# Optimization experiments

Hardware: AMD Instinct MI355X
Metric: run time of the kernel (lower is better)

Reference implementation:

```python
import jax, jax.numpy as jnp
import numpy as np

K = 9          # neighbors kept after dilation
DILATION = 2   # top-k runs with K*DILATION then strided slice
EPS = 1e-12    # F.normalize eps


def setup_inputs() -> dict:
    key = jax.random.key(0)
    # x: [B, C, N, 1] feature map over N points with C channels
    x = jax.random.normal(key, (2, 64, 8192, 1), dtype=jnp.float32)
    return {"x": x}


def reference(x):
    k_total = K * DILATION
    # L2-normalize along channel dim (F.normalize(x, p=2, dim=1))
    norm = jnp.sqrt(jnp.sum(x * x, axis=1, keepdims=True))
    xn = x / jnp.maximum(norm, EPS)
    # [B, C, N, 1] -> [B, N, C]
    pts = jnp.transpose(jnp.squeeze(xn, -1), (0, 2, 1))
    B, N, _ = pts.shape
    # pairwise squared distances: ||xi||^2 - 2 xi.xj + ||xj||^2  -> [B, N, N]
    sq = jnp.sum(pts * pts, axis=-1, keepdims=True)            # [B, N, 1]
    dist = sq - 2.0 * jnp.einsum('bnc,bmc->bnm', pts, pts) + jnp.swapaxes(sq, 1, 2)
    # k nearest = top-k of negated distance (matches torch.topk(-dist, k))
    _, nn_idx = jax.lax.top_k(-dist, k_total)                  # [B, N, k_total] int32
    center_idx = jnp.broadcast_to(jnp.arange(N, dtype=nn_idx.dtype)[None, :, None],
                                  (B, N, k_total))
    edge_index = jnp.stack([nn_idx, center_idx], axis=0)       # [2, B, N, k_total]
    # dilation (non-stochastic path): strided slice over neighbor dim
    return edge_index[:, :, :, ::DILATION]                     # [2, B, N, K]
```

## Files before the change

### kernel.cpp

```cpp
#include <hip/hip_runtime.h>


#define NPTS  8192
#define CHN   64
#define NB    2
#define KF    18
#define KC    8
#define KM    20
#define KOUT  9
#define NPART 4
#define TPB   32

typedef unsigned u32;
typedef unsigned short u16;
typedef unsigned long long u64;
typedef __attribute__((ext_vector_type(4))) unsigned u32x4;
typedef __attribute__((ext_vector_type(8))) short bf16x8;
typedef __attribute__((ext_vector_type(4))) float f32x4;

__device__ __forceinline__ u32 umin32(u32 a, u32 b) { return a < b ? a : b; }
__device__ __forceinline__ u32 umax32(u32 a, u32 b) { return a > b ? a : b; }

__device__ __forceinline__ u32 mono32(float f) {
  const u32 u = __float_as_uint(f);
  const u32 s = (u32)((int)u >> 31);
  return u ^ (s | 0x80000000u);
}

__device__ __forceinline__ u32 med3u(u32 a, u32 b, u32 c) {
  u32 r;
  asm("v_med3_u32 %0, %1, %2, %3" : "=v"(r) : "v"(a), "v"(b), "v"(c));
  return r;
}

template <int KK>
__device__ __forceinline__ void insmm(u32 key, u32 (&d)[KK]) {
#pragma unroll
  for (int k = KK - 1; k >= 1; --k) d[k] = med3u(d[k - 1], d[k], key);
  d[0] = umin32(d[0], key);
}

template <int KK>
__device__ __forceinline__ void ins64(u64 key, u64 (&d)[KK]) {
  if (key < d[KK - 1]) {
#pragma unroll
    for (int k = KK - 1; k >= 1; --k) {
      const bool up = d[k - 1] > key;
      const bool here = (!up) && (d[k] > key);
      d[k] = up ? d[k - 1] : (here ? key : d[k]);
    }
    if (d[0] > key) d[0] = key;
  }
}

__device__ __forceinline__ void gload_lds16(const u32* g, u32* l) {
  __builtin_amdgcn_global_load_lds(
      (const __attribute__((address_space(1))) u32*)g,
      (__attribute__((address_space(3))) u32*)l, 16, 0, 0);
}

__device__ __forceinline__ void np_normalize(const float* __restrict__ xb,
                                             float (&v)[CHN]) {
  float ss = 0.f;
#pragma unroll
  for (int c = 0; c < CHN; ++c) {
    v[c] = xb[(size_t)c * NPTS];
    ss = __fadd_rn(ss, __fmul_rn(v[c], v[c]));
  }
  const float den = fmaxf(__fsqrt_rn(ss), 1e-12f);
#pragma unroll
  for (int c = 0; c < CHN; ++c) v[c] = __fdiv_rn(v[c], den);
}

__global__ __launch_bounds__(128) void prep_kernel(
    const float* __restrict__ x, u32* __restrict__ hib, u32* __restrict__ lob,
    float* __restrict__ sq) {
  const int b = blockIdx.x >> 6;
  const int n = ((blockIdx.x & 63) << 7) + threadIdx.x;
  float v[CHN];
  np_normalize(x + (size_t)b * CHN * NPTS + n, v);
  float r[8];
#pragma unroll
  for (int j = 0; j < 8; ++j) r[j] = __fmul_rn(v[j], v[j]);
#pragma unroll
  for (int blk = 1; blk < 8; ++blk)
#pragma unroll
    for (int j = 0; j < 8; ++j)
      r[j] = __fadd_rn(r[j], __fmul_rn(v[8 * blk + j], v[8 * blk + j]));
  const float t0 = __fadd_rn(r[0], r[1]);
  const float t1 = __fadd_rn(r[2], r[3]);
  const float t2 = __fadd_rn(r[4], r[5]);
  const float t3 = __fadd_rn(r[6], r[7]);
  sq[(b << 13) + n] = __fadd_rn(__fadd_rn(t0, t1), __fadd_rn(t2, t3));
  u32* hd = hib + (size_t)((b << 13) + n) * 32;
  u32* ld = lob + (size_t)((b << 13) + n) * 32;
  const int key = n & 7;
#pragma unroll
  for (int q = 0; q < 8; ++q) {
    u32 h[4], l[4];
#pragma unroll
    for (int p2 = 0; p2 < 4; ++p2) {
      const float a = v[8 * q + 2 * p2];
      const float c = v[8 * q + 2 * p2 + 1];
      const u32 ba = __float_as_uint(a), bc = __float_as_uint(c);
      const float la = a - __uint_as_float(ba & 0xffff0000u);
      const float lc = c - __uint_as_float(bc & 0xffff0000u);
      h[p2] = __builtin_amdgcn_perm(bc, ba, 0x07060302u);
      l[p2] = __builtin_amdgcn_perm(__float_as_uint(lc), __float_as_uint(la),
                                    0x07060302u);
    }
    const int pq = (q ^ key) << 2;
    *(u32x4*)(hd + pq) = (u32x4){h[0], h[1], h[2], h[3]};
    *(u32x4*)(ld + pq) = (u32x4){l[0], l[1], l[2], l[3]};
  }
}

__global__ __launch_bounds__(128) void prep2_kernel(
    const float* __restrict__ x, float* __restrict__ pts) {
  const int b = blockIdx.x >> 6;
  const int n = ((blockIdx.x & 63) << 7) + threadIdx.x;
  float v[CHN];
  np_normalize(x + (size_t)b * CHN * NPTS + n, v);
  float4* dst = (float4*)(pts + (size_t)(b * NPTS + n) * CHN);
#pragma unroll
  for (int u = 0; u < 16; ++u)
    dst[u] = make_float4(v[4 * u], v[4 * u + 1], v[4 * u + 2], v[4 * u + 3]);
}

__global__ __launch_bounds__(256, 3) void knn_part_kernel(
    const u32* __restrict__ hib, const u32* __restrict__ lob,
    const float* __restrict__ sq, u16* __restrict__ cand) {
  __shared__ __align__(16) u32 pp[2][4096];
  __shared__ float sqp[2][64];

  const int tid = threadIdx.x;
  const int vb = ((blockIdx.x & 7) << 7) + (blockIdx.x >> 3);
  const int part = vb >> 8;
  const int w = vb & 255;
  const int b = w >> 7;
  const int qbase = (w & 127) << 6;
  const int t_lo = part << 5;
  const u32* __restrict__ hb_ = hib + ((size_t)b << 18);
  const u32* __restrict__ lb_ = lob + ((size_t)b << 18);
  const float* __restrict__ sqb = sq + (b << 13);

  const int lane = tid & 63, wid = tid >> 6;
  const int qoff = (wid & 1) << 5;
  const int moff = (wid >> 1) << 5;
  const int l15 = lane & 15;
  const int h4 = lane >> 4;
  const int sw = l15 & 7;

  {
    const u32* sH = hb_ + ((size_t)t_lo << 11);
    const u32* sL = lb_ + ((size_t)t_lo << 11);
    gload_lds16(sH + (tid << 2), pp[0] + (tid << 2));
    gload_lds16(sH + 1024 + (tid << 2), pp[0] + 1024 + (tid << 2));
    gload_lds16(sL + (tid << 2), pp[0] + 2048 + (tid << 2));
    gload_lds16(sL + 1024 + (tid << 2), pp[0] + 3072 + (tid << 2));
    if (tid < 64) sqp[0][tid] = (sqb[(t_lo << 6) + tid] + 2.f) * 0.5f;
  }

  bf16x8 ah[2][2], al[2][2];
#pragma unroll
  for (int g = 0; g < 2; ++g)
#pragma unroll
    for (int s = 0; s < 2; ++s) {
      const int row = qbase + qoff + (g << 4) + l15;
      const int off = row * 32 + ((((s << 2) + h4) ^ sw) << 2);
      u32x4 hv = *(const u32x4*)(hb_ + off);
      u32x4 lv = *(const u32x4*)(lb_ + off);
      hv.x ^= 0x80008000u; hv.y ^= 0x80008000u;
      hv.z ^= 0x80008000u; hv.w ^= 0x80008000u;
      lv.x ^= 0x80008000u; lv.y ^= 0x80008000u;
      lv.z ^= 0x80008000u; lv.w ^= 0x80008000u;
      ah[g][s] = __builtin_bit_cast(bf16x8, hv);
      al[g][s] = __builtin_bit_cast(bf16x8, lv);
    }
  __syncthreads();

  u32 d[2][4][KC];
#pragma unroll
  for (int g = 0; g < 2; ++g)
#pragma unroll
    for (int i = 0; i < 4; ++i)
#pragma unroll
      for (int k = 0; k < KC; ++k) d[g][i][k] = 0xffffffffu;

  for (int tau = 0; tau < TPB; ++tau) {
    const int cur = tau & 1;
    float sqv = 0.f;
    const bool more = (tau + 1) < TPB;
    if (more) {
      const u32* sH = hb_ + ((size_t)(t_lo + tau + 1) << 11);
      const u32* sL = lb_ + ((size_t)(t_lo + tau + 1) << 11);
      u32* wp = pp[cur ^ 1];
      gload_lds16(sH + (tid << 2), wp + (tid << 2));
      gload_lds16(sH + 1024 + (tid << 2), wp + 1024 + (tid << 2));
      gload_lds16(sL + (tid << 2), wp + 2048 + (tid << 2));
      gload_lds16(sL + 1024 + (tid << 2), wp + 3072 + (tid << 2));
      if (tid < 64) sqv = sqb[((t_lo + tau + 1) << 6) + tid];
    }
    const u32* ppc = pp[cur];
#pragma unroll
    for (int f = 0; f < 2; ++f) {
      const int m_l = moff + (f << 4) + l15;
      const float sqm = sqp[cur][m_l];
      f32x4 acc[2];
      acc[0] = (f32x4){sqm, sqm, sqm, sqm};
      acc[1] = acc[0];
#pragma unroll
      for (int s = 0; s < 2; ++s) {
        const u32* hp = ppc + m_l * 32 + ((((s << 2) + h4) ^ sw) << 2);
        const bf16x8 bh = __builtin_bit_cast(bf16x8, *(const u32x4*)hp);
        const bf16x8 bl = __builtin_bit_cast(bf16x8, *(const u32x4*)(hp + 2048));
        acc[0] = __builtin_amdgcn_mfma_f32_16x16x32_bf16(ah[0][s], bh, acc[0], 0, 0, 0);
        acc[1] = __builtin_amdgcn_mfma_f32_16x16x32_bf16(ah[1][s], bh, acc[1], 0, 0, 0);
        acc[0] = __builtin_amdgcn_mfma_f32_16x16x32_bf16(al[0][s], bh, acc[0], 0, 0, 0);
        acc[1] = __builtin_amdgcn_mfma_f32_16x16x32_bf16(al[1][s], bh, acc[1], 0, 0, 0);
        acc[0] = __builtin_amdgcn_mfma_f32_16x16x32_bf16(ah[0][s], bl, acc[0], 0, 0, 0);
        acc[1] = __builtin_amdgcn_mfma_f32_16x16x32_bf16(ah[1][s], bl, acc[1], 0, 0, 0);
      }
      const u32 lidx = (u32)((tau << 6) + m_l);
#pragma unroll
      for (int g = 0; g < 2; ++g)
#pragma unroll
        for (int i = 0; i < 4; ++i) {
          const u32 keyv = (__float_as_uint(acc[g][i]) & 0xfffff000u) | lidx;
          insmm<KC>(keyv, d[g][i]);
        }
    }
    if (more && tid < 64) sqp[cur ^ 1][tid] = (sqv + 2.f) * 0.5f;
    __syncthreads();
  }

  u32* mg = &pp[0][0];
  const int stream = ((wid >> 1) << 4) + l15;
  const int rcb = ((wid & 1) << 4) + (h4 << 2);
#pragma unroll
  for (int chunk = 0; chunk < 2; ++chunk) {
#pragma unroll
    for (int i = 0; i < 4; ++i) {
      u32* wr = mg + ((rcb + i) * 32 + stream) * 8;
      u32x4 a, c;
      a.x = d[chunk][i][0]; a.y = d[chunk][i][1];
      a.z = d[chunk][i][2]; a.w = d[chunk][i][3];
      c.x = d[chunk][i][4]; c.y = d[chunk][i][5];
      c.z = d[chunk][i][6]; c.w = d[chunk][i][7];
      *(u32x4*)wr = a;
      *(u32x4*)(wr + 4) = c;
    }
    __syncthreads();
    {
      const int rowc = tid >> 3, oct = tid & 7;
      u32* base = mg + rowc * 256 + oct * 32;
      u32 m1[14];
#pragma unroll
      for (int k = 0; k < 14; ++k) m1[k] = 0xffffffffu;
#pragma unroll
      for (int j = 0; j < 8; ++j) {
        const u32x4 k4 = *(const u32x4*)(base + (j << 2));
        insmm<14>(k4.x, m1);
        insmm<14>(k4.y, m1);
        insmm<14>(k4.z, m1);
        insmm<14>(k4.w, m1);
      }
#pragma unroll
      for (int k = 0; k < 14; ++k) base[k] = m1[k];
    }
    __syncthreads();
    if (tid < 64) {
      const int rowc = tid >> 1, half = tid & 1;
      u32* rb = mg + rowc * 256 + half * 128;
      u32 m2[KM];
#pragma unroll
      for (int k = 0; k < KM; ++k) m2[k] = 0xffffffffu;
#pragma unroll
      for (int o = 0; o < 4; ++o) {
        const u32* p = rb + o * 32;
        for (int j = 0; j < 14; ++j) insmm<KM>(p[j], m2);
      }
#pragma unroll
      for (int k = 0; k < KM; ++k) rb[k] = m2[k];
    }
    __syncthreads();
    if (tid < 32) {
      u32 m3[KM];
#pragma unroll
      for (int k = 0; k < KM; ++k) m3[k] = 0xffffffffu;
      const u32* p0 = mg + tid * 256;
      for (int j = 0; j < KM; ++j) insmm<KM>(p0[j], m3);
      const u32* p1 = mg + tid * 256 + 128;
      for (int j = 0; j < KM; ++j) insmm<KM>(p1[j], m3);
      const int row = ((tid >> 4) << 5) + (chunk << 4) + (tid & 15);
      const int rg = (b << 13) + qbase + row;
      u16* cw = cand + (size_t)rg * (NPART * KM) + part * KM;
#pragma unroll
      for (int k = 0; k < KM; ++k)
        cw[k] = (u16)((part << 11) + (m3[k] & 0xfffu));
    }
    __syncthreads();
  }
}

__global__ __launch_bounds__(512) void finalize_kernel(
    const float* __restrict__ pts, const float* __restrict__ sq,
    const u16* __restrict__ cand, int* __restrict__ out) {
  __shared__ u64 ex[64 * 81];
  __shared__ u64 hf[128 * 19];
  const int tid = threadIdx.x;
  const int rl = tid >> 3, sub = tid & 7;
  const int row = (blockIdx.x << 6) + rl;
  const int b = row >> 13;
  const float sqn = sq[row];
  const float* __restrict__ qrow = pts + ((size_t)row << 6);
  const float* __restrict__ sqb = sq + (b << 13);
  const u16* __restrict__ cr = cand + (size_t)row * 80 + sub * 10;
  u64* exw = ex + rl * 81 + sub * 10;
#pragma unroll 2
  for (int j = 0; j < 10; ++j) {
    const int ix = cr[j];
    const float* __restrict__ pv = pts + ((size_t)((b << 13) + ix) << 6);
    float dot = 0.f;
#pragma unroll
    for (int c = 0; c < CHN; ++c)
      dot = __fadd_rn(dot, __fmul_rn(qrow[c], pv[c]));
    const float dist =
        __fadd_rn(__fsub_rn(sqn, __fmul_rn(2.0f, dot)), sqb[ix]);
    exw[j] = ((u64)mono32(dist) << 32) | (u32)ix;
  }
  __syncthreads();
  if (tid < 128) {
    const int r2 = tid >> 1, hv = tid & 1;
    u64 m18[KF];
#pragma unroll
    for (int k = 0; k < KF; ++k) m18[k] = ~0ull;
    const u64* p = ex + r2 * 81 + hv * 40;
    for (int j = 0; j < 40; ++j) ins64<KF>(p[j], m18);
    u64* wr = hf + tid * 19;
#pragma unroll
    for (int k = 0; k < KF; ++k) wr[k] = m18[k];
  }
  __syncthreads();
  if (tid < 64) {
    u64 m18[KF];
#pragma unroll
    for (int k = 0; k < KF; ++k) m18[k] = ~0ull;
    const u64* p0 = hf + (tid << 1) * 19;
    const u64* p1 = hf + ((tid << 1) + 1) * 19;
    for (int j = 0; j < KF; ++j) ins64<KF>(p0[j], m18);
    for (int j = 0; j < KF; ++j) ins64<KF>(p1[j], m18);
    const int row2 = (blockIdx.x << 6) + tid;
    int* o0 = out + (size_t)row2 * KOUT;
    int* o1 = o0 + NB * NPTS * KOUT;
#pragma unroll
    for (int k = 0; k < KOUT; ++k) {
      o0[k] = (int)(m18[2 * k] & 0xffffffffu);
      o1[k] = row2 & 8191;
    }
  }
}

extern "C" void kernel_launch(void* const* d_in, const int* in_sizes, int n_in,
                              void* d_out, int out_size, void* d_ws, size_t ws_size,
                              hipStream_t stream) {
  const float* x = (const float*)d_in[0];
  u32* hib = (u32*)d_ws;
  u32* lob = hib + (size_t)NB * NPTS * 32;
  float* pts = (float*)d_ws;
  float* sqg = (float*)(hib + (size_t)NB * NPTS * 64);
  u16* cand = (u16*)(sqg + NB * NPTS);
  int* out = (int*)d_out;
  prep_kernel<<<dim3(128), dim3(128), 0, stream>>>(x, hib, lob, sqg);
  knn_part_kernel<<<dim3(1024), dim3(256), 0, stream>>>(hib, lob, sqg, cand);
  prep2_kernel<<<dim3(128), dim3(128), 0, stream>>>(x, pts);
  finalize_kernel<<<dim3(256), dim3(512), 0, stream>>>(pts, sqg, cand, out);
}
```

Before: 228.3 us.

## Fuse pts write into prep kernel, widen grid, batch finalize dot products

The prep kernel now also writes the normalized fp32 points into a separate workspace region when the workspace is large enough. This removes the prep2 launch and its second pass over x. Both prep kernels now use 64-thread blocks across 256 blocks to spread over more CUs. The finalize kernel computes all 10 candidate dot products together in an interleaved channel loop, which exposes more memory-level parallelism at the cost of more registers.

Measured after the change: 238.1 us. +4.3%, slower.

```diff
diff --git a/kernel.cpp b/kernel.cpp
--- a/kernel.cpp
+++ b/kernel.cpp
@@ -19,7 +19,6 @@
 typedef __attribute__((ext_vector_type(4))) float f32x4;
 
 __device__ __forceinline__ u32 umin32(u32 a, u32 b) { return a < b ? a : b; }
-__device__ __forceinline__ u32 umax32(u32 a, u32 b) { return a > b ? a : b; }
 
 __device__ __forceinline__ u32 mono32(float f) {
   const u32 u = __float_as_uint(f);
@@ -72,11 +71,12 @@
   for (int c = 0; c < CHN; ++c) v[c] = __fdiv_rn(v[c], den);
 }
 
-__global__ __launch_bounds__(128) void prep_kernel(
+__global__ __launch_bounds__(64) void prep_kernel(
     const float* __restrict__ x, u32* __restrict__ hib, u32* __restrict__ lob,
-    float* __restrict__ sq) {
-  const int b = blockIdx.x >> 6;
-  const int n = ((blockIdx.x & 63) << 7) + threadIdx.x;
+    float* __restrict__ sq, float* __restrict__ pts ) {
+  const int g = (blockIdx.x << 6) + threadIdx.x;
+  const int b = g >> 13;
+  const int n = g & 8191;
   float v[CHN];
   np_normalize(x + (size_t)b * CHN * NPTS + n, v);
   float r[8];
@@ -91,9 +91,9 @@
   const float t1 = __fadd_rn(r[2], r[3]);
   const float t2 = __fadd_rn(r[4], r[5]);
   const float t3 = __fadd_rn(r[6], r[7]);
-  sq[(b << 13) + n] = __fadd_rn(__fadd_rn(t0, t1), __fadd_rn(t2, t3));
-  u32* hd = hib + (size_t)((b << 13) + n) * 32;
-  u32* ld = lob + (size_t)((b << 13) + n) * 32;
+  sq[g] = __fadd_rn(__fadd_rn(t0, t1), __fadd_rn(t2, t3));
+  u32* hd = hib + (size_t)g * 32;
+  u32* ld = lob + (size_t)g * 32;
   const int key = n & 7;
 #pragma unroll
   for (int q = 0; q < 8; ++q) {
@@ -113,15 +113,22 @@
     *(u32x4*)(hd + pq) = (u32x4){h[0], h[1], h[2], h[3]};
     *(u32x4*)(ld + pq) = (u32x4){l[0], l[1], l[2], l[3]};
   }
-}
-
-__global__ __launch_bounds__(128) void prep2_kernel(
+  if (pts) {
+    float4* dst = (float4*)(pts + (size_t)g * CHN);
+#pragma unroll
+    for (int u = 0; u < 16; ++u)
+      dst[u] = make_float4(v[4 * u], v[4 * u + 1], v[4 * u + 2], v[4 * u + 3]);
+  }
+}
+
+__global__ __launch_bounds__(64) void prep2_kernel(
     const float* __restrict__ x, float* __restrict__ pts) {
-  const int b = blockIdx.x >> 6;
-  const int n = ((blockIdx.x & 63) << 7) + threadIdx.x;
+  const int g = (blockIdx.x << 6) + threadIdx.x;
+  const int b = g >> 13;
+  const int n = g & 8191;
   float v[CHN];
   np_normalize(x + (size_t)b * CHN * NPTS + n, v);
-  float4* dst = (float4*)(pts + (size_t)(b * NPTS + n) * CHN);
+  float4* dst = (float4*)(pts + (size_t)g * CHN);
 #pragma unroll
   for (int u = 0; u < 16; ++u)
     dst[u] = make_float4(v[4 * u], v[4 * u + 1], v[4 * u + 2], v[4 * u + 3]);
@@ -316,18 +323,28 @@
   const float* __restrict__ qrow = pts + ((size_t)row << 6);
   const float* __restrict__ sqb = sq + (b << 13);
   const u16* __restrict__ cr = cand + (size_t)row * 80 + sub * 10;
+  int ixs[10];
+  const float* pv[10];
+  float dot[10];
+#pragma unroll
+  for (int j = 0; j < 10; ++j) {
+    ixs[j] = cr[j];
+    pv[j] = pts + ((size_t)((b << 13) + ixs[j]) << 6);
+    dot[j] = 0.f;
+  }
+#pragma unroll
+  for (int c = 0; c < CHN; ++c) {
+    const float qc = qrow[c];
+#pragma unroll
+    for (int j = 0; j < 10; ++j)
+      dot[j] = __fadd_rn(dot[j], __fmul_rn(qc, pv[j][c]));
+  }
   u64* exw = ex + rl * 81 + sub * 10;
-#pragma unroll 2
+#pragma unroll
   for (int j = 0; j < 10; ++j) {
-    const int ix = cr[j];
-    const float* __restrict__ pv = pts + ((size_t)((b << 13) + ix) << 6);
-    float dot = 0.f;
-#pragma unroll
-    for (int c = 0; c < CHN; ++c)
-      dot = __fadd_rn(dot, __fmul_rn(qrow[c], pv[c]));
     const float dist =
-        __fadd_rn(__fsub_rn(sqn, __fmul_rn(2.0f, dot)), sqb[ix]);
-    exw[j] = ((u64)mono32(dist) << 32) | (u32)ix;
+        __fadd_rn(__fsub_rn(sqn, __fmul_rn(2.0f, dot[j])), sqb[ixs[j]]);
+    exw[j] = ((u64)mono32(dist) << 32) | (u32)ixs[j];
   }
   __syncthreads();
   if (tid < 128) {
@@ -367,12 +384,26 @@
   const float* x = (const float*)d_in[0];
   u32* hib = (u32*)d_ws;
   u32* lob = hib + (size_t)NB * NPTS * 32;
-  float* pts = (float*)d_ws;
   float* sqg = (float*)(hib + (size_t)NB * NPTS * 64);
   u16* cand = (u16*)(sqg + NB * NPTS);
   int* out = (int*)d_out;
-  prep_kernel<<<dim3(128), dim3(128), 0, stream>>>(x, hib, lob, sqg);
-  knn_part_kernel<<<dim3(1024), dim3(256), 0, stream>>>(hib, lob, sqg, cand);
-  prep2_kernel<<<dim3(128), dim3(128), 0, stream>>>(x, pts);
-  finalize_kernel<<<dim3(256), dim3(512), 0, stream>>>(pts, sqg, cand, out);
-}
+
+  const size_t base_bytes =
+      (size_t)NB * NPTS * 64 * 4 + (size_t)NB * NPTS * 4 +
+      (size_t)NB * NPTS * NPART * KM * 2;
+  const size_t pts_bytes = (size_t)NB * NPTS * CHN * 4;
+  const bool big = ws_size >= base_bytes + pts_bytes + 1024;
+
+  if (big) {
+    float* pts = (float*)((char*)d_ws + base_bytes);
+    prep_kernel<<<dim3(256), dim3(64), 0, stream>>>(x, hib, lob, sqg, pts);
+    knn_part_kernel<<<dim3(1024), dim3(256), 0, stream>>>(hib, lob, sqg, cand);
+    finalize_kernel<<<dim3(256), dim3(512), 0, stream>>>(pts, sqg, cand, out);
+  } else {
+    float* pts = (float*)d_ws;
+    prep_kernel<<<dim3(256), dim3(64), 0, stream>>>(x, hib, lob, sqg, nullptr);
+    knn_part_kernel<<<dim3(1024), dim3(256), 0, stream>>>(hib, lob, sqg, cand);
+    prep2_kernel<<<dim3(256), dim3(64), 0, stream>>>(x, pts);
+    finalize_kernel<<<dim3(256), dim3(512), 0, stream>>>(pts, sqg, cand, out);
+  }
+}
```

## Give each wave private double-buffered LDS tiles and drop per-iteration block barriers

Applied to the files above, without the earlier changes.

The main kNN loop now has each wave stage its own 32-row slice of the candidate tile into a private double-buffered LDS region. It waits only on its own outstanding async loads (vmcnt) instead of calling __syncthreads every iteration. Squared norms are loaded straight into registers rather than through shared memory. The cost is duplicated LDS traffic (two waves load the same m-rows), a doubled LDS footprint, and launch bounds lowered from 3 to 2 blocks per CU.

Measured after the change: 235.1 us. 3.0% more time.

```diff
diff --git a/kernel.cpp b/kernel.cpp
--- a/kernel.cpp
+++ b/kernel.cpp
@@ -19,7 +19,6 @@
 typedef __attribute__((ext_vector_type(4))) float f32x4;
 
 __device__ __forceinline__ u32 umin32(u32 a, u32 b) { return a < b ? a : b; }
-__device__ __forceinline__ u32 umax32(u32 a, u32 b) { return a > b ? a : b; }
 
 __device__ __forceinline__ u32 mono32(float f) {
   const u32 u = __float_as_uint(f);
@@ -77,6 +76,7 @@
     float* __restrict__ sq) {
   const int b = blockIdx.x >> 6;
   const int n = ((blockIdx.x & 63) << 7) + threadIdx.x;
+  const int g = (b << 13) + n;
   float v[CHN];
   np_normalize(x + (size_t)b * CHN * NPTS + n, v);
   float r[8];
@@ -91,9 +91,9 @@
   const float t1 = __fadd_rn(r[2], r[3]);
   const float t2 = __fadd_rn(r[4], r[5]);
   const float t3 = __fadd_rn(r[6], r[7]);
-  sq[(b << 13) + n] = __fadd_rn(__fadd_rn(t0, t1), __fadd_rn(t2, t3));
-  u32* hd = hib + (size_t)((b << 13) + n) * 32;
-  u32* ld = lob + (size_t)((b << 13) + n) * 32;
+  sq[g] = __fadd_rn(__fadd_rn(t0, t1), __fadd_rn(t2, t3));
+  u32* hd = hib + (size_t)g * 32;
+  u32* ld = lob + (size_t)g * 32;
   const int key = n & 7;
 #pragma unroll
   for (int q = 0; q < 8; ++q) {
@@ -121,17 +121,16 @@
   const int n = ((blockIdx.x & 63) << 7) + threadIdx.x;
   float v[CHN];
   np_normalize(x + (size_t)b * CHN * NPTS + n, v);
-  float4* dst = (float4*)(pts + (size_t)(b * NPTS + n) * CHN);
+  float4* dst = (float4*)(pts + (size_t)((b << 13) + n) * CHN);
 #pragma unroll
   for (int u = 0; u < 16; ++u)
     dst[u] = make_float4(v[4 * u], v[4 * u + 1], v[4 * u + 2], v[4 * u + 3]);
 }
 
-__global__ __launch_bounds__(256, 3) void knn_part_kernel(
+__global__ __launch_bounds__(256, 2) void knn_part_kernel(
     const u32* __restrict__ hib, const u32* __restrict__ lob,
     const float* __restrict__ sq, u16* __restrict__ cand) {
-  __shared__ __align__(16) u32 pp[2][4096];
-  __shared__ float sqp[2][64];
+  __shared__ __align__(16) u32 pw[4][2][2048];
 
   const int tid = threadIdx.x;
   const int vb = ((blockIdx.x & 7) << 7) + (blockIdx.x >> 3);
@@ -151,15 +150,25 @@
   const int h4 = lane >> 4;
   const int sw = l15 & 7;
 
-  {
-    const u32* sH = hb_ + ((size_t)t_lo << 11);
-    const u32* sL = lb_ + ((size_t)t_lo << 11);
-    gload_lds16(sH + (tid << 2), pp[0] + (tid << 2));
-    gload_lds16(sH + 1024 + (tid << 2), pp[0] + 1024 + (tid << 2));
-    gload_lds16(sL + (tid << 2), pp[0] + 2048 + (tid << 2));
-    gload_lds16(sL + 1024 + (tid << 2), pp[0] + 3072 + (tid << 2));
-    if (tid < 64) sqp[0][tid] = (sqb[(t_lo << 6) + tid] + 2.f) * 0.5f;
-  }
+  const int lofs = lane << 2;
+#define STAGE(BUF, TILE)                                                     \
+  {                                                                          \
+    const u32* sH_ = hb_ + ((size_t)(TILE) << 11) + (moff << 5);             \
+    const u32* sL_ = lb_ + ((size_t)(TILE) << 11) + (moff << 5);             \
+    u32* bp_ = &pw[wid][(BUF)][0];                                           \
+    gload_lds16(sH_ + lofs, bp_ + lofs);                                     \
+    gload_lds16(sH_ + 256 + lofs, bp_ + 256 + lofs);                         \
+    gload_lds16(sH_ + 512 + lofs, bp_ + 512 + lofs);                         \
+    gload_lds16(sH_ + 768 + lofs, bp_ + 768 + lofs);                         \
+    gload_lds16(sL_ + lofs, bp_ + 1024 + lofs);                              \
+    gload_lds16(sL_ + 256 + lofs, bp_ + 1280 + lofs);                        \
+    gload_lds16(sL_ + 512 + lofs, bp_ + 1536 + lofs);                        \
+    gload_lds16(sL_ + 768 + lofs, bp_ + 1792 + lofs);                        \
+  }
+
+  STAGE(0, t_lo)
+  float sqn0 = sqb[(t_lo << 6) + moff + l15];
+  float sqn1 = sqb[(t_lo << 6) + moff + 16 + l15];
 
   bf16x8 ah[2][2], al[2][2];
 #pragma unroll
@@ -177,7 +186,8 @@
       ah[g][s] = __builtin_bit_cast(bf16x8, hv);
       al[g][s] = __builtin_bit_cast(bf16x8, lv);
     }
-  __syncthreads();
+  asm volatile("s_waitcnt vmcnt(0)" ::: "memory");
+  __builtin_amdgcn_sched_barrier(0);
 
   u32 d[2][4][KC];
 #pragma unroll
@@ -189,31 +199,30 @@
 
   for (int tau = 0; tau < TPB; ++tau) {
     const int cur = tau & 1;
-    float sqv = 0.f;
-    const bool more = (tau + 1) < TPB;
-    if (more) {
-      const u32* sH = hb_ + ((size_t)(t_lo + tau + 1) << 11);
-      const u32* sL = lb_ + ((size_t)(t_lo + tau + 1) << 11);
-      u32* wp = pp[cur ^ 1];
-      gload_lds16(sH + (tid << 2), wp + (tid << 2));
-      gload_lds16(sH + 1024 + (tid << 2), wp + 1024 + (tid << 2));
-      gload_lds16(sL + (tid << 2), wp + 2048 + (tid << 2));
-      gload_lds16(sL + 1024 + (tid << 2), wp + 3072 + (tid << 2));
-      if (tid < 64) sqv = sqb[((t_lo + tau + 1) << 6) + tid];
-    }
-    const u32* ppc = pp[cur];
+    const float sq0 = sqn0, sq1 = sqn1;
+    if (tau + 1 < TPB) {
+      STAGE(cur ^ 1, t_lo + tau + 1)
+      sqn0 = sqb[((t_lo + tau + 1) << 6) + moff + l15];
+      sqn1 = sqb[((t_lo + tau + 1) << 6) + moff + 16 + l15];
+      asm volatile("s_waitcnt vmcnt(10)" ::: "memory");
+    } else {
+      asm volatile("s_waitcnt vmcnt(0)" ::: "memory");
+    }
+    __builtin_amdgcn_sched_barrier(0);
+
+    const u32* ppc = &pw[wid][cur][0];
 #pragma unroll
     for (int f = 0; f < 2; ++f) {
-      const int m_l = moff + (f << 4) + l15;
-      const float sqm = sqp[cur][m_l];
+      const float sqm = ((f ? sq1 : sq0) + 2.f) * 0.5f;
+      const int rloc = (f << 4) + l15;
       f32x4 acc[2];
       acc[0] = (f32x4){sqm, sqm, sqm, sqm};
       acc[1] = acc[0];
 #pragma unroll
       for (int s = 0; s < 2; ++s) {
-        const u32* hp = ppc + m_l * 32 + ((((s << 2) + h4) ^ sw) << 2);
+        const u32* hp = ppc + rloc * 32 + ((((s << 2) + h4) ^ sw) << 2);
         const bf16x8 bh = __builtin_bit_cast(bf16x8, *(const u32x4*)hp);
-        const bf16x8 bl = __builtin_bit_cast(bf16x8, *(const u32x4*)(hp + 2048));
+        const bf16x8 bl = __builtin_bit_cast(bf16x8, *(const u32x4*)(hp + 1024));
         acc[0] = __builtin_amdgcn_mfma_f32_16x16x32_bf16(ah[0][s], bh, acc[0], 0, 0, 0);
         acc[1] = __builtin_amdgcn_mfma_f32_16x16x32_bf16(ah[1][s], bh, acc[1], 0, 0, 0);
         acc[0] = __builtin_amdgcn_mfma_f32_16x16x32_bf16(al[0][s], bh, acc[0], 0, 0, 0);
@@ -221,7 +230,7 @@
         acc[0] = __builtin_amdgcn_mfma_f32_16x16x32_bf16(ah[0][s], bl, acc[0], 0, 0, 0);
         acc[1] = __builtin_amdgcn_mfma_f32_16x16x32_bf16(ah[1][s], bl, acc[1], 0, 0, 0);
       }
-      const u32 lidx = (u32)((tau << 6) + m_l);
+      const u32 lidx = (u32)((tau << 6) + moff + rloc);
 #pragma unroll
       for (int g = 0; g < 2; ++g)
 #pragma unroll
@@ -230,11 +239,11 @@
           insmm<KC>(keyv, d[g][i]);
         }
     }
-    if (more && tid < 64) sqp[cur ^ 1][tid] = (sqv + 2.f) * 0.5f;
-    __syncthreads();
-  }
-
-  u32* mg = &pp[0][0];
+  }
+#undef STAGE
+  __syncthreads();
+
+  u32* mg = &pw[0][0][0];
   const int stream = ((wid >> 1) << 4) + l15;
   const int rcb = ((wid & 1) << 4) + (h4 << 2);
 #pragma unroll
```
